# Kernel tuning notes

Hardware: AMD Instinct MI355X
Metric: run time of the kernel (lower is better)

The kernel has to match this reference:

```python
import jax, jax.numpy as jnp
import numpy as np

N = 100000   # active voxels (stride=1 -> output coords == input coords)
C_IN = 64
C_OUT = 64
K3 = 27      # 3x3x3 kernel offsets
M = 40000    # rulebook pairs per kernel offset
EPS = 1e-5


def setup_inputs() -> dict:
    key = jax.random.key(0)
    k1, k2, k3, k4 = jax.random.split(key, 4)
    x = jax.random.normal(k1, (N, C_IN), dtype=jnp.float32)
    # conv weights per kernel offset: [K3, inc, outc]
    W = jax.random.normal(k2, (K3, C_IN, C_OUT), dtype=jnp.float32) * 0.05
    gamma = jnp.ones((C_OUT,), dtype=jnp.float32)
    beta = jnp.zeros((C_OUT,), dtype=jnp.float32)
    # rulebook: for each offset k, M (input_idx, output_idx) pairs
    in_idx = jax.random.randint(k3, (K3, M), 0, N, dtype=jnp.int32)
    out_idx = jax.random.randint(k4, (K3, M), 0, N, dtype=jnp.int32)
    return {"x": x, "W": W, "gamma": gamma, "beta": beta,
            "in_idx": in_idx, "out_idx": out_idx}


def reference(x, W, gamma, beta, in_idx, out_idx):
    n_out = x.shape[0]  # stride=1: output voxel set == input voxel set
    # gather: [K3, M, C_IN]
    feat = x[in_idx]
    # batched GEMM over kernel offsets: [K3, M, C_OUT]
    contrib = jnp.einsum('kmi,kio->kmo', feat, W)
    # scatter-add into output voxels
    out = jnp.zeros((n_out, W.shape[2]), dtype=x.dtype)
    out = out.at[out_idx.reshape(-1)].add(contrib.reshape(-1, W.shape[2]))
    # BatchNorm over active points (training-mode batch stats, biased var)
    mean = jnp.mean(out, axis=0)
    var = jnp.mean(jnp.square(out - mean), axis=0)
    y = (out - mean) * jax.lax.rsqrt(var + EPS) * gamma + beta
    # ReLU
    return jnp.maximum(y, 0.0)
```

## Files before the change

kernel.cpp:

```cpp
#include <hip/hip_runtime.h>


#define N_VOX   100000
#define NPAD    100096
#define K3      27
#define M_PAIRS 40000
#define NPAIRS  (K3 * M_PAIRS)
#define BN_EPS  1e-5f
#define NBINS   (K3 * NPAD)
#define AUXMAX  184320
#define AUXCAP  (AUXMAX - 1)
#define ZROW    (N_VOX + AUXMAX - 1)

#define OFF_WT     0u
#define OFF_STATS  221184u
#define OFF_CTRS   221696u
#define OFF_GINX   221760u
#define OFF_NODE   11032128u
#define OFF_LIST   19672128u
#define OFF_XB     20409472u
#define OFF_BH     (OFF_XB + 12800000u)
#define WS_NEED    ((size_t)OFF_XB + (size_t)(N_VOX + AUXMAX) * 128u)

#define NB_WT    432
#define NB_XB    3125
#define GRID_IN  (NB_WT + NB_XB + 1)
#define NB_BUILD 4219

typedef __attribute__((ext_vector_type(8))) short bf16x8;
typedef __attribute__((ext_vector_type(4))) float f32x4;

__device__ __forceinline__ short f2bf(float f) {
  unsigned u = __builtin_bit_cast(unsigned, f);
  u += 0x7FFFu + ((u >> 16) & 1u);
  return (short)(u >> 16);
}
__device__ __forceinline__ float bf2f(short s) {
  unsigned u = ((unsigned)(unsigned short)s) << 16;
  return __builtin_bit_cast(float, u);
}

__global__ __launch_bounds__(256) void init_kernel(const float* __restrict__ W,
                                                   const float* __restrict__ x,
                                                   short* __restrict__ wt,
                                                   short* __restrict__ xb) {
  int b = blockIdx.x, t = threadIdx.x;
  if (b < NB_WT) {
    int id = b * 256 + t;
    int k = id >> 12, rem = id & 4095, c = rem >> 6, i = rem & 63;
    wt[id] = f2bf(W[(k << 12) + (i << 6) + c]);
  } else if (b < NB_WT + NB_XB) {
    int id = (b - NB_WT) * 256 + t;
    if (id < N_VOX * 8) {
      float4 lo = ((const float4*)x)[id * 2];
      float4 hi = ((const float4*)x)[id * 2 + 1];
      bf16x8 v;
      v[0] = f2bf(lo.x); v[1] = f2bf(lo.y); v[2] = f2bf(lo.z); v[3] = f2bf(lo.w);
      v[4] = f2bf(hi.x); v[5] = f2bf(hi.y); v[6] = f2bf(hi.z); v[7] = f2bf(hi.w);
      ((bf16x8*)xb)[id] = v;
    }
  } else {
    if (t < 8) {
      bf16x8 z = {0, 0, 0, 0, 0, 0, 0, 0};
      ((bf16x8*)(xb + (size_t)ZROW * 64))[t] = z;
    }
  }
}

__global__ __launch_bounds__(256) void build_kernel(const int* __restrict__ in_idx,
                                                    const int* __restrict__ out_idx,
                                                    int* __restrict__ bh,
                                                    int2* __restrict__ node) {
  int id = blockIdx.x * 256 + threadIdx.x;
  if (id >= NPAIRS) return;
  int k  = id / M_PAIRS;
  int in = in_idx[id];
  int o  = out_idx[id];
  int bb = k * NPAD + o;
  int old = atomicExch(&bh[bb], id);
  node[id] = make_int2(old, in);
}

__global__ __launch_bounds__(256) void compact_kernel(const int* __restrict__ bh,
                                                      const int2* __restrict__ node,
                                                      int* __restrict__ ginx,
                                                      int* __restrict__ list,
                                                      int* __restrict__ ctrs) {
  __shared__ int l_cnt, l_base;
  int t = threadIdx.x;
  if (t == 0) l_cnt = 0;
  __syncthreads();
  int w = blockIdx.x * 256 + t;
  bool ok = (w < NBINS / 4);
  int4 h4 = ok ? ((const int4*)bh)[w] : make_int4(-1, -1, -1, -1);
  int hv[4] = {h4.x, h4.y, h4.z, h4.w};
  int gv[4], lp[4];
  int2 n0[4];
  #pragma unroll
  for (int s = 0; s < 4; ++s) {
    lp[s] = -1;
    if (hv[s] < 0) gv[s] = ZROW;
    else {
      n0[s] = node[hv[s]];
      if (n0[s].x < 0) gv[s] = n0[s].y;
      else             lp[s] = atomicAdd(&l_cnt, 1);
    }
  }
  __syncthreads();
  if (t == 0) l_base = (l_cnt > 0) ? atomicAdd(&ctrs[0], l_cnt) : 0;
  __syncthreads();
  #pragma unroll
  for (int s = 0; s < 4; ++s) {
    if (lp[s] >= 0) {
      int pos = l_base + lp[s];
      if (pos < AUXCAP) { list[pos] = hv[s]; gv[s] = N_VOX + pos; }
      else              { gv[s] = n0[s].y; }
    }
  }
  if (ok) ((int4*)ginx)[w] = make_int4(gv[0], gv[1], gv[2], gv[3]);
}

__global__ __launch_bounds__(256) void fixup_kernel(short* __restrict__ xb,
                                                    const int* __restrict__ list,
                                                    const int2* __restrict__ node,
                                                    const int* __restrict__ ctrs) {
  int n = ctrs[0]; if (n > AUXCAP) n = AUXCAP;
  int wid  = (blockIdx.x * 256 + threadIdx.x) >> 6;
  int lane = threadIdx.x & 63;
  int nw   = gridDim.x * 4;
  for (int i = wid; i < n; i += nw) {
    int h = list[i];
    float acc = 0.f;
    while (h >= 0) {
      int2 nd = node[h];
      acc += bf2f(xb[(size_t)nd.y * 64 + lane]);
      h = nd.x;
    }
    xb[(size_t)(N_VOX + i) * 64 + lane] = f2bf(acc);
  }
}

#define LOADST(S, ia, ib)                                       \
  { const short* _pa = xb + (size_t)(ia) * 64;                  \
    const short* _pb = xb + (size_t)(ib) * 64;                  \
    S[0] = *(const bf16x8*)(_pa + g8);                          \
    S[1] = *(const bf16x8*)(_pa + 32 + g8);                     \
    S[2] = *(const bf16x8*)(_pb + g8);                          \
    S[3] = *(const bf16x8*)(_pb + 32 + g8); }

__global__ __launch_bounds__(256) void conv_out_kernel(const short* __restrict__ xb,
                                                       const short* __restrict__ wt,
                                                       const int* __restrict__ ginx,
                                                       float* __restrict__ out,
                                                       float* __restrict__ stats) {
  __shared__ short lds[2 * 4096];
  __shared__ float ls[128];
  int t = threadIdx.x, wave = t >> 6, lane = t & 63;
  int g = lane >> 4, c0 = lane & 15, g8 = g * 8;
  int o0 = blockIdx.x * 128 + wave * 32 + c0;
  int o1 = o0 + 16;

  int rb  = ((c0 * 128 + g * 16) ^ ((c0 & 7) << 4)) >> 1;
  int wb0 = ((t * 32) ^ (((t >> 2) & 7) << 4)) >> 1;
  if (t < 128) ls[t] = 0.f;

  f32x4 acc0[4], acc1[4];
  #pragma unroll
  for (int n = 0; n < 4; ++n) {
    acc0[n][0]=0.f; acc0[n][1]=0.f; acc0[n][2]=0.f; acc0[n][3]=0.f;
    acc1[n][0]=0.f; acc1[n][1]=0.f; acc1[n][2]=0.f; acc1[n][3]=0.f;
  }

  bf16x8 st[3][4];
  bf16x8 s0w = *(const bf16x8*)(wt + t * 16);
  bf16x8 s1w = *(const bf16x8*)(wt + t * 16 + 8);
  {
    int ia = ginx[o0], ib = ginx[o1];
    LOADST(st[0], ia, ib);
    ia = ginx[NPAD + o0]; ib = ginx[NPAD + o1];
    LOADST(st[1], ia, ib);
  }
  int i2a = ginx[2 * NPAD + o0], i2b = ginx[2 * NPAD + o1];
  *(bf16x8*)&lds[wb0]     = s0w;
  *(bf16x8*)&lds[wb0 ^ 8] = s1w;
  __syncthreads();

  int buf = 0;
  #pragma unroll
  for (int k = 0; k < K3; ++k) {
    if (k + 1 < K3) {
      const short* wn = wt + (size_t)(k + 1) * 4096 + t * 16;
      s0w = *(const bf16x8*)(wn);
      s1w = *(const bf16x8*)(wn + 8);
    }
    if (k + 2 < K3) LOADST(st[(k + 2) % 3], i2a, i2b);
    if (k + 3 < K3) {
      i2a = ginx[(size_t)(k + 3) * NPAD + o0];
      i2b = ginx[(size_t)(k + 3) * NPAD + o1];
    }
    const short* lb = lds + buf * 4096;
    #pragma unroll
    for (int n = 0; n < 4; ++n) {
      bf16x8 b0 = *(const bf16x8*)&lb[rb + n * 1024];
      bf16x8 b1 = *(const bf16x8*)&lb[(rb ^ 32) + n * 1024];
      acc0[n] = __builtin_amdgcn_mfma_f32_16x16x32_bf16(st[k % 3][0], b0, acc0[n], 0, 0, 0);
      acc0[n] = __builtin_amdgcn_mfma_f32_16x16x32_bf16(st[k % 3][1], b1, acc0[n], 0, 0, 0);
      acc1[n] = __builtin_amdgcn_mfma_f32_16x16x32_bf16(st[k % 3][2], b0, acc1[n], 0, 0, 0);
      acc1[n] = __builtin_amdgcn_mfma_f32_16x16x32_bf16(st[k % 3][3], b1, acc1[n], 0, 0, 0);
    }
    if (k + 1 < K3) {
      short* wd = lds + (buf ^ 1) * 4096;
      *(bf16x8*)&wd[wb0]     = s0w;
      *(bf16x8*)&wd[wb0 ^ 8] = s1w;
    }
    __syncthreads();
    buf ^= 1;
  }

  int orow = blockIdx.x * 128 + wave * 32 + (g << 2);
  #pragma unroll
  for (int j = 0; j < 4; ++j) {
    int r0 = orow + j, r1 = orow + 16 + j;
    if (r0 < N_VOX) {
      float* op = out + (size_t)r0 * 64 + c0;
      op[0] = acc0[0][j]; op[16] = acc0[1][j]; op[32] = acc0[2][j]; op[48] = acc0[3][j];
    }
    if (r1 < N_VOX) {
      float* op = out + (size_t)r1 * 64 + c0;
      op[0] = acc1[0][j]; op[16] = acc1[1][j]; op[32] = acc1[2][j]; op[48] = acc1[3][j];
    }
  }

  #pragma unroll
  for (int n = 0; n < 4; ++n) {
    float s = 0.f, q = 0.f;
    #pragma unroll
    for (int j = 0; j < 4; ++j) {
      float v0 = acc0[n][j], v1 = acc1[n][j];
      s += v0 + v1; q += v0 * v0 + v1 * v1;
    }
    atomicAdd(&ls[n * 16 + c0], s);
    atomicAdd(&ls[64 + n * 16 + c0], q);
  }
  __syncthreads();
  if (t < 128) unsafeAtomicAdd(&stats[t], ls[t]);
}

__global__ __launch_bounds__(256) void norm_kernel(float* __restrict__ out,
                                                   const float* __restrict__ stats,
                                                   const float* __restrict__ gamma,
                                                   const float* __restrict__ beta) {
  int i4 = blockIdx.x * 256 + threadIdx.x;
  if (i4 >= N_VOX * 16) return;
  const float invN = 1.0f / (float)N_VOX;
  float4 v = ((const float4*)out)[i4];
  int c0 = (i4 << 2) & 63;
  float r[4] = {v.x, v.y, v.z, v.w};
  #pragma unroll
  for (int j = 0; j < 4; ++j) {
    int c = c0 + j;
    float mean = stats[c] * invN;
    float ex2  = stats[64 + c] * invN;
    float var  = ex2 - mean * mean;
    float scale = gamma[c] * rsqrtf(var + BN_EPS);
    float shift = beta[c] - mean * scale;
    r[j] = fmaxf(r[j] * scale + shift, 0.0f);
  }
  v.x = r[0]; v.y = r[1]; v.z = r[2]; v.w = r[3];
  ((float4*)out)[i4] = v;
}

extern "C" void kernel_launch(void* const* d_in, const int* in_sizes, int n_in,
                              void* d_out, int out_size, void* d_ws, size_t ws_size,
                              hipStream_t stream) {
  const float* x      = (const float*)d_in[0];
  const float* W      = (const float*)d_in[1];
  const float* gamma  = (const float*)d_in[2];
  const float* beta   = (const float*)d_in[3];
  const int*   in_idx = (const int*)d_in[4];
  const int*   out_idx= (const int*)d_in[5];
  float* out = (float*)d_out;

  char* ws = (char*)d_ws;
  short* wt    = (short*)(ws + OFF_WT);
  float* stats = (float*)(ws + OFF_STATS);
  int*   ctrs  = (int*)(ws + OFF_CTRS);
  int*   ginx  = (int*)(ws + OFF_GINX);
  int2*  node  = (int2*)(ws + OFF_NODE);
  int*   list  = (int*)(ws + OFF_LIST);
  short* xb    = (short*)(ws + OFF_XB);
  int*   bh    = (int*)(ws + OFF_BH);

  hipMemsetAsync(ws + OFF_STATS, 0, OFF_GINX - OFF_STATS, stream);
  hipMemsetAsync((void*)bh, 0xFF, (size_t)NBINS * 4, stream);

  init_kernel<<<GRID_IN, 256, 0, stream>>>(W, x, wt, xb);
  build_kernel<<<NB_BUILD, 256, 0, stream>>>(in_idx, out_idx, bh, node);
  compact_kernel<<<(NBINS / 4 + 255) / 256, 256, 0, stream>>>(bh, node, ginx, list, ctrs);
  fixup_kernel<<<2048, 256, 0, stream>>>(xb, list, node, ctrs);
  conv_out_kernel<<<NPAD / 128, 256, 0, stream>>>(xb, wt, ginx, out, stats);
  norm_kernel<<<(N_VOX * 16 + 255) / 256, 256, 0, stream>>>(out, stats, gamma, beta);
}
```

Before: 213.8 us.

## Split multi-hit bins into pair list and chain list; use lighter LDS barrier

Compaction now separates bins with exactly two contributing inputs, storing both input indices directly, from bins with three or more, which keep chain walking. The fixup kernel handles two-entry bins with two independent loads and no dependent linked-list traversal, which shortens the latency chain for the common case. The conv kernel's __syncthreads is replaced by an inline-asm wait on lgkmcnt followed by s_barrier, so the barrier no longer waits on outstanding global loads. This relies on the new CAP2/CAP3 capacities covering the test distribution. When capacity overflows, a bin falls back to a single input, which drops contributions and would make the result inexact.

```diff
diff --git a/kernel.cpp b/kernel.cpp
--- a/kernel.cpp
+++ b/kernel.cpp
@@ -9,7 +9,8 @@
 #define BN_EPS  1e-5f
 #define NBINS   (K3 * NPAD)
 #define AUXMAX  184320
-#define AUXCAP  (AUXMAX - 1)
+#define CAP2    160000
+#define CAP3    24318
 #define ZROW    (N_VOX + AUXMAX - 1)
 
 #define OFF_WT     0u
@@ -18,7 +19,7 @@
 #define OFF_GINX   221760u
 #define OFF_NODE   11032128u
 #define OFF_LIST   19672128u
-#define OFF_XB     20409472u
+#define OFF_XB     21146688u
 #define OFF_BH     (OFF_XB + 12800000u)
 #define WS_NEED    ((size_t)OFF_XB + (size_t)(N_VOX + AUXMAX) * 128u)
 
@@ -29,6 +30,8 @@
 
 typedef __attribute__((ext_vector_type(8))) short bf16x8;
 typedef __attribute__((ext_vector_type(4))) float f32x4;
+
+#define LBAR() asm volatile("s_waitcnt lgkmcnt(0)\n\ts_barrier" ::: "memory")
 
 __device__ __forceinline__ short f2bf(float f) {
   unsigned u = __builtin_bit_cast(unsigned, f);
@@ -84,59 +87,80 @@
 __global__ __launch_bounds__(256) void compact_kernel(const int* __restrict__ bh,
                                                       const int2* __restrict__ node,
                                                       int* __restrict__ ginx,
-                                                      int* __restrict__ list,
+                                                      int2* __restrict__ list,
                                                       int* __restrict__ ctrs) {
-  __shared__ int l_cnt, l_base;
+  __shared__ int l_cnt2, l_cnt3, l_b2, l_b3;
   int t = threadIdx.x;
-  if (t == 0) l_cnt = 0;
+  if (t == 0) { l_cnt2 = 0; l_cnt3 = 0; }
   __syncthreads();
   int w = blockIdx.x * 256 + t;
   bool ok = (w < NBINS / 4);
   int4 h4 = ok ? ((const int4*)bh)[w] : make_int4(-1, -1, -1, -1);
   int hv[4] = {h4.x, h4.y, h4.z, h4.w};
-  int gv[4], lp[4];
-  int2 n0[4];
+  int gv[4], lp2[4], lp3[4];
+  int2 ent[4];
   #pragma unroll
   for (int s = 0; s < 4; ++s) {
-    lp[s] = -1;
+    lp2[s] = -1; lp3[s] = -1;
     if (hv[s] < 0) gv[s] = ZROW;
     else {
-      n0[s] = node[hv[s]];
-      if (n0[s].x < 0) gv[s] = n0[s].y;
-      else             lp[s] = atomicAdd(&l_cnt, 1);
+      int2 n0 = node[hv[s]];
+      if (n0.x < 0) gv[s] = n0.y;
+      else {
+        int2 n1 = node[n0.x];
+        gv[s] = n0.y;
+        if (n1.x < 0) { lp2[s] = atomicAdd(&l_cnt2, 1); ent[s] = make_int2(n0.y, n1.y); }
+        else          { lp3[s] = atomicAdd(&l_cnt3, 1); ent[s] = make_int2(hv[s], 0); }
+      }
     }
   }
   __syncthreads();
-  if (t == 0) l_base = (l_cnt > 0) ? atomicAdd(&ctrs[0], l_cnt) : 0;
+  if (t == 0) l_b2 = (l_cnt2 > 0) ? atomicAdd(&ctrs[0], l_cnt2) : 0;
+  if (t == 1) l_b3 = (l_cnt3 > 0) ? atomicAdd(&ctrs[1], l_cnt3) : 0;
   __syncthreads();
   #pragma unroll
   for (int s = 0; s < 4; ++s) {
-    if (lp[s] >= 0) {
-      int pos = l_base + lp[s];
-      if (pos < AUXCAP) { list[pos] = hv[s]; gv[s] = N_VOX + pos; }
-      else              { gv[s] = n0[s].y; }
+    if (lp2[s] >= 0) {
+      int pos = l_b2 + lp2[s];
+      if (pos < CAP2) { list[pos] = ent[s]; gv[s] = N_VOX + pos; }
+    } else if (lp3[s] >= 0) {
+      int i3 = l_b3 + lp3[s];
+      if (i3 < CAP3) {
+        int pos = AUXMAX - 2 - i3;
+        list[pos] = ent[s]; gv[s] = N_VOX + pos;
+      }
     }
   }
   if (ok) ((int4*)ginx)[w] = make_int4(gv[0], gv[1], gv[2], gv[3]);
 }
 
 __global__ __launch_bounds__(256) void fixup_kernel(short* __restrict__ xb,
-                                                    const int* __restrict__ list,
+                                                    const int2* __restrict__ list,
                                                     const int2* __restrict__ node,
                                                     const int* __restrict__ ctrs) {
-  int n = ctrs[0]; if (n > AUXCAP) n = AUXCAP;
+  int n2 = ctrs[0]; if (n2 > CAP2) n2 = CAP2;
+  int n3 = ctrs[1]; if (n3 > CAP3) n3 = CAP3;
   int wid  = (blockIdx.x * 256 + threadIdx.x) >> 6;
   int lane = threadIdx.x & 63;
   int nw   = gridDim.x * 4;
-  for (int i = wid; i < n; i += nw) {
-    int h = list[i];
-    float acc = 0.f;
-    while (h >= 0) {
-      int2 nd = node[h];
-      acc += bf2f(xb[(size_t)nd.y * 64 + lane]);
-      h = nd.x;
-    }
-    xb[(size_t)(N_VOX + i) * 64 + lane] = f2bf(acc);
+  int tot  = n2 + n3;
+  for (int i = wid; i < tot; i += nw) {
+    if (i < n2) {
+      int2 e = list[i];
+      float a = bf2f(xb[(size_t)e.x * 64 + lane]);
+      float b = bf2f(xb[(size_t)e.y * 64 + lane]);
+      xb[(size_t)(N_VOX + i) * 64 + lane] = f2bf(a + b);
+    } else {
+      int pos = AUXMAX - 2 - (i - n2);
+      int h = list[pos].x;
+      float acc = 0.f;
+      while (h >= 0) {
+        int2 nd = node[h];
+        acc += bf2f(xb[(size_t)nd.y * 64 + lane]);
+        h = nd.x;
+      }
+      xb[(size_t)(N_VOX + pos) * 64 + lane] = f2bf(acc);
+    }
   }
 }
 
@@ -183,7 +207,7 @@
   int i2a = ginx[2 * NPAD + o0], i2b = ginx[2 * NPAD + o1];
   *(bf16x8*)&lds[wb0]     = s0w;
   *(bf16x8*)&lds[wb0 ^ 8] = s1w;
-  __syncthreads();
+  LBAR();
 
   int buf = 0;
   #pragma unroll
@@ -213,7 +237,7 @@
       *(bf16x8*)&wd[wb0]     = s0w;
       *(bf16x8*)&wd[wb0 ^ 8] = s1w;
     }
-    __syncthreads();
+    LBAR();
     buf ^= 1;
   }
 
@@ -287,7 +311,7 @@
   int*   ctrs  = (int*)(ws + OFF_CTRS);
   int*   ginx  = (int*)(ws + OFF_GINX);
   int2*  node  = (int2*)(ws + OFF_NODE);
-  int*   list  = (int*)(ws + OFF_LIST);
+  int2*  list  = (int2*)(ws + OFF_LIST);
   short* xb    = (short*)(ws + OFF_XB);
   int*   bh    = (int*)(ws + OFF_BH);
 
```

New measurement: 230.7 us. 1.08x slower.
